# Kernel tuning notes

Measured on AMD Instinct MI355X. Metric: run time of the kernel, lower is better.

Reference implementation:

```python
import jax, jax.numpy as jnp
import numpy as np

B, T, C = 4, 2048, 1024
H, D = 16, 64          # n_head, head_size; H*D == C
FF = 4 * C             # compute_layer_scaling * n_embed
EPS = 1e-5


def layernorm(x, g, b):
    mu = jnp.mean(x, axis=-1, keepdims=True)
    var = jnp.var(x, axis=-1, keepdims=True)
    return (x - mu) * jax.lax.rsqrt(var + EPS) * g + b


def setup_inputs() -> dict:
    key = jax.random.key(0)
    ks = jax.random.split(key, 12)
    s_c = 1.0 / np.sqrt(C)
    s_ff = 1.0 / np.sqrt(FF)
    return {
        "x": jax.random.normal(ks[0], (B, T, C), dtype=jnp.float32),
        # per-head Q/K/V weights, stacked: [H, C, D] (Linear with bias=False)
        "Wq": jax.random.normal(ks[1], (H, C, D), dtype=jnp.float32) * s_c,
        "Wk": jax.random.normal(ks[2], (H, C, D), dtype=jnp.float32) * s_c,
        "Wv": jax.random.normal(ks[3], (H, C, D), dtype=jnp.float32) * s_c,
        "Wproj": jax.random.normal(ks[4], (C, C), dtype=jnp.float32) * s_c,
        "bproj": jnp.zeros((C,), dtype=jnp.float32),
        "W1": jax.random.normal(ks[5], (C, FF), dtype=jnp.float32) * s_c,
        "b1": jnp.zeros((FF,), dtype=jnp.float32),
        "W2": jax.random.normal(ks[6], (FF, FF), dtype=jnp.float32) * s_ff,
        "b2": jnp.zeros((FF,), dtype=jnp.float32),
        "W3": jax.random.normal(ks[7], (FF, C), dtype=jnp.float32) * s_ff,
        "b3": jnp.zeros((C,), dtype=jnp.float32),
        "ln1_g": jnp.ones((C,), dtype=jnp.float32),
        "ln1_b": jnp.zeros((C,), dtype=jnp.float32),
        "ln2_g": jnp.ones((C,), dtype=jnp.float32),
        "ln2_b": jnp.zeros((C,), dtype=jnp.float32),
    }


def reference(x, Wq, Wk, Wv, Wproj, bproj, W1, b1, W2, b2, W3, b3,
              ln1_g, ln1_b, ln2_g, ln2_b):
    # --- multi-head causal self-attention (pre-LN) ---
    h = layernorm(x, ln1_g, ln1_b)
    q = jnp.einsum("btc,hcd->bhtd", h, Wq)
    k = jnp.einsum("btc,hcd->bhtd", h, Wk)
    v = jnp.einsum("btc,hcd->bhtd", h, Wv)
    # NOTE: original scales by n_embed**-0.5 (C from x.shape), not head_size
    scores = jnp.einsum("bhtd,bhsd->bhts", q, k) * (C ** -0.5)
    causal = jnp.tril(jnp.ones((T, T), dtype=bool))
    scores = jnp.where(causal, scores, -jnp.inf)
    wei = jax.nn.softmax(scores, axis=-1)          # dropout p=0 -> identity
    attn = jnp.einsum("bhts,bhsd->bhtd", wei, v)
    attn = attn.transpose(0, 2, 1, 3).reshape(B, T, C)  # concat heads
    x = x + attn @ Wproj + bproj
    # --- feed-forward (pre-LN): C -> FF -> relu -> FF -> relu -> C ---
    h2 = layernorm(x, ln2_g, ln2_b)
    h2 = jax.nn.relu(h2 @ W1 + b1)
    h2 = jax.nn.relu(h2 @ W2 + b2)
    x = x + h2 @ W3 + b3
    return x
```

## Files before the change

kernel.cpp:

```cpp
#include <hip/hip_runtime.h>

typedef __bf16 bf16;
typedef bf16  bf16x8 __attribute__((ext_vector_type(8)));
typedef bf16  bf16x4 __attribute__((ext_vector_type(4)));
typedef float f32x4  __attribute__((ext_vector_type(4)));

#define T_SEQ 2048

__device__ __forceinline__ void gload_lds16(const bf16* g, bf16* l) {
    __builtin_amdgcn_global_load_lds(
        (const __attribute__((address_space(1))) unsigned int*)g,
        (__attribute__((address_space(3))) unsigned int*)l,
        16, 0, 0);
}

#define VMCNT(n) asm volatile("s_waitcnt vmcnt(" #n ")" ::: "memory")
#define BAR() do { asm volatile("" ::: "memory"); __builtin_amdgcn_s_barrier(); \
                   asm volatile("" ::: "memory"); } while (0)

__global__ __launch_bounds__(256) void transpose_f32_bf16(
    const float* __restrict__ in, bf16* __restrict__ out, int R, int Cc, int ldo)
{
    __shared__ float tile[32][33];
    const int bx = blockIdx.x * 32;
    const int by = blockIdx.y * 32;
    const long bi = (long)blockIdx.z * R * Cc;
    const long bo = (long)blockIdx.z * Cc * ldo;
    const int tx = threadIdx.x, ty = threadIdx.y;
#pragma unroll
    for (int i = 0; i < 4; ++i)
        tile[ty + i * 8][tx] = in[bi + (long)(by + ty + i * 8) * Cc + bx + tx];
    __syncthreads();
#pragma unroll
    for (int i = 0; i < 4; ++i)
        out[bo + (long)(bx + ty + i * 8) * ldo + by + tx] = (bf16)tile[tx][ty + i * 8];
}

__global__ __launch_bounds__(256) void ln_kernel(
    const float* __restrict__ x, const float* __restrict__ g,
    const float* __restrict__ bb, bf16* __restrict__ out)
{
    const long row = blockIdx.x;
    const int tid = threadIdx.x;
    const float4 v = ((const float4*)(x + row * 1024))[tid];
    float s  = v.x + v.y + v.z + v.w;
    float s2 = v.x * v.x + v.y * v.y + v.z * v.z + v.w * v.w;
#pragma unroll
    for (int off = 32; off >= 1; off >>= 1) {
        s  += __shfl_xor(s,  off, 64);
        s2 += __shfl_xor(s2, off, 64);
    }
    __shared__ float red[8];
    const int wid = tid >> 6;
    if ((tid & 63) == 0) { red[wid] = s; red[4 + wid] = s2; }
    __syncthreads();
    s  = red[0] + red[1] + red[2] + red[3];
    s2 = red[4] + red[5] + red[6] + red[7];
    const float mu   = s * (1.f / 1024.f);
    const float rstd = rsqrtf(s2 * (1.f / 1024.f) - mu * mu + 1e-5f);
    const float4 gv = ((const float4*)g)[tid];
    const float4 bv = ((const float4*)bb)[tid];
    bf16x4 ov;
    ov[0] = (bf16)((v.x - mu) * rstd * gv.x + bv.x);
    ov[1] = (bf16)((v.y - mu) * rstd * gv.y + bv.y);
    ov[2] = (bf16)((v.z - mu) * rstd * gv.z + bv.z);
    ov[3] = (bf16)((v.w - mu) * rstd * gv.w + bv.w);
    *(bf16x4*)(out + row * 1024 + tid * 4) = ov;
}

template <int MODE>
__global__ __launch_bounds__(256) void gemm_bt(
    const bf16* __restrict__ A, const bf16* __restrict__ Bt,
    const float* __restrict__ bias, const float* __restrict__ resid,
    void* __restrict__ outp, int M, int N, int K)
{
    __shared__ __align__(16) bf16 As[128 * 32];
    __shared__ __align__(16) bf16 Bs[128 * 32];
    const int tid = threadIdx.x;
    const int wid = tid >> 6, lane = tid & 63;
    const int wr = wid >> 1, wc = wid & 1;
    const int fr = lane & 15, fq = lane >> 4;
    const long bm = blockIdx.x, bn = blockIdx.y;

    const int c0   = wid * 2;
    const int row0 = c0 * 16 + (lane >> 2);
    const int kk8  = (lane & 3) * 8;
    const bf16* gA0 = A  + ((long)(bm * 128 + row0)) * K + kk8;
    const bf16* gA1 = gA0 + 16l * K;
    const bf16* gB0 = Bt + ((long)(bn * 128 + row0)) * K + kk8;
    const bf16* gB1 = gB0 + 16l * K;
    bf16* lA0 = &As[c0 * 512];
    bf16* lA1 = &As[(c0 + 1) * 512];
    bf16* lB0 = &Bs[c0 * 512];
    bf16* lB1 = &Bs[(c0 + 1) * 512];

    f32x4 acc[4][4];
#pragma unroll
    for (int m = 0; m < 4; ++m)
#pragma unroll
        for (int n = 0; n < 4; ++n) acc[m][n] = {0.f, 0.f, 0.f, 0.f};

    for (int k0 = 0; k0 < K; k0 += 32) {
        __syncthreads();
        gload_lds16(gA0 + k0, lA0);
        gload_lds16(gA1 + k0, lA1);
        gload_lds16(gB0 + k0, lB0);
        gload_lds16(gB1 + k0, lB1);
        __syncthreads();
        bf16x8 af[4], bfr[4];
#pragma unroll
        for (int m = 0; m < 4; ++m)
            af[m] = *(const bf16x8*)&As[(wr * 64 + m * 16 + fr) * 32 + fq * 8];
#pragma unroll
        for (int n = 0; n < 4; ++n)
            bfr[n] = *(const bf16x8*)&Bs[(wc * 64 + n * 16 + fr) * 32 + fq * 8];
#pragma unroll
        for (int m = 0; m < 4; ++m)
#pragma unroll
            for (int n = 0; n < 4; ++n)
                acc[m][n] = __builtin_amdgcn_mfma_f32_16x16x32_bf16(
                    af[m], bfr[n], acc[m][n], 0, 0, 0);
    }

#pragma unroll
    for (int m = 0; m < 4; ++m) {
        const long row0o = bm * 128 + wr * 64 + m * 16 + fq * 4;
#pragma unroll
        for (int n = 0; n < 4; ++n) {
            const long col = bn * 128 + wc * 64 + n * 16 + fr;
            const float bv = (MODE == 0) ? 0.f : bias[col];
#pragma unroll
            for (int j = 0; j < 4; ++j) {
                const long row = row0o + j;
                float v = acc[m][n][j] + bv;
                if (MODE == 1) v = fmaxf(v, 0.f);
                if (MODE == 2) {
                    v += resid[row * N + col];
                    ((float*)outp)[row * N + col] = v;
                } else {
                    ((bf16*)outp)[row * N + col] = (bf16)v;
                }
            }
        }
    }
}

#define LOADA(BUFP, QM) do {                                                   \
    const char* ab_ = (BUFP) + (size_t)((wr * 64 + (QM) * 128 + fr) * 128);    \
    _Pragma("unroll") for (int m_ = 0; m_ < 4; ++m_) {                         \
        af[m_][0] = *(const bf16x8*)(ab_ + m_ * 2048 + so0);                   \
        af[m_][1] = *(const bf16x8*)(ab_ + m_ * 2048 + so1); } } while (0)

#define LOADB(BUFP, QN) do {                                                   \
    const char* bb_ = (BUFP) + (size_t)((wc * 32 + (QN) * 128 + fr) * 128);    \
    _Pragma("unroll") for (int n_ = 0; n_ < 2; ++n_) {                         \
        bfv[n_][0] = *(const bf16x8*)(bb_ + n_ * 2048 + so0);                  \
        bfv[n_][1] = *(const bf16x8*)(bb_ + n_ * 2048 + so1); } } while (0)

#define MMA(ACC) do { __builtin_amdgcn_s_setprio(1);                           \
    _Pragma("unroll") for (int m_ = 0; m_ < 4; ++m_)                           \
    _Pragma("unroll") for (int n_ = 0; n_ < 2; ++n_) {                         \
        ACC[m_][n_] = __builtin_amdgcn_mfma_f32_16x16x32_bf16(                 \
            af[m_][0], bfv[n_][0], ACC[m_][n_], 0, 0, 0);                      \
        ACC[m_][n_] = __builtin_amdgcn_mfma_f32_16x16x32_bf16(                 \
            af[m_][1], bfv[n_][1], ACC[m_][n_], 0, 0, 0); }                    \
    __builtin_amdgcn_s_setprio(0); } while (0)

#define TILE_BODY(PRE) do {                                                    \
    const char* abuf = cAs + ((size_t)cur << 15);                              \
    const char* bbuf = cBs + ((size_t)cur << 15);                              \
    const long kn = (long)(k + 1) * 64;                                        \
    LOADA(abuf, 0);                                                            \
    LOADB(bbuf, 0);                                                            \
    if (PRE) { stageA(nxt, 0, kn); VMCNT(4); } else { VMCNT(2); }              \
    BAR(); MMA(a00); BAR();                                                    \
    LOADB(bbuf, 1);                                                            \
    if (PRE) { stageB(nxt, 0, kn); VMCNT(4); } else { VMCNT(0); }              \
    BAR(); MMA(a01); BAR();                                                    \
    LOADA(abuf, 1);                                                            \
    if (PRE) { stageB(nxt, 1, kn); }                                           \
    BAR(); MMA(a11); BAR();                                                    \
    LOADB(bbuf, 0);                                                            \
    if (PRE) { stageA(nxt, 1, kn); VMCNT(4); }                                 \
    BAR(); MMA(a10); BAR(); } while (0)

template <int MODE>
__global__ __launch_bounds__(512, 2) void gemm256(
    const bf16* __restrict__ A, const bf16* __restrict__ Bt,
    const float* __restrict__ bias, const float* __restrict__ resid,
    void* __restrict__ outp, int M, int N, int K, int nbn)
{
    extern __shared__ __align__(16) char smem[];
    char* cAs = smem;
    char* cBs = smem + 65536;

    const int tid = threadIdx.x;
    const int wid = tid >> 6, lane = tid & 63;
    const int wr = wid >> 2, wc = wid & 3;
    const int fr = lane & 15, fq = lane >> 4;

    const int nwg = gridDim.x;
    const int cpx = nwg >> 3;
    const int b0  = blockIdx.x;
    const int bid = (b0 & 7) * cpx + (b0 >> 3);
    const long bm = bid / nbn, bn = bid % nbn;
    const long bmrow = bm * 256, bnrow = bn * 256;

    const int srow0 = wid * 8 + (lane >> 3);
    const int sslot = (lane & 7) ^ (lane >> 3);
    auto stageA = [&](int buf, int h, long kt) {
        const bf16* g = A + (size_t)(bmrow + h * 128 + srow0) * K + kt + sslot * 8;
        char* l = cAs + ((size_t)buf << 15) + h * 16384 + (size_t)wid * 1024;
        gload_lds16(g, (bf16*)l);
        gload_lds16(g + (size_t)64 * K, (bf16*)(l + 8192));
    };
    auto stageB = [&](int buf, int h, long kt) {
        const bf16* g = Bt + (size_t)(bnrow + h * 128 + srow0) * K + kt + sslot * 8;
        char* l = cBs + ((size_t)buf << 15) + h * 16384 + (size_t)wid * 1024;
        gload_lds16(g, (bf16*)l);
        gload_lds16(g + (size_t)64 * K, (bf16*)(l + 8192));
    };

    const int sx  = fr & 7;
    const int so0 = ((fq) ^ sx) * 16;
    const int so1 = ((4 + fq) ^ sx) * 16;

    bf16x8 af[4][2], bfv[2][2];
    f32x4 a00[4][2], a01[4][2], a11[4][2], a10[4][2];
#pragma unroll
    for (int m = 0; m < 4; ++m)
#pragma unroll
        for (int n = 0; n < 2; ++n) {
            a00[m][n] = {0.f, 0.f, 0.f, 0.f}; a01[m][n] = {0.f, 0.f, 0.f, 0.f};
            a11[m][n] = {0.f, 0.f, 0.f, 0.f}; a10[m][n] = {0.f, 0.f, 0.f, 0.f};
        }

    stageA(0, 0, 0); stageB(0, 0, 0); stageB(0, 1, 0); stageA(0, 1, 0);
    VMCNT(4);
    BAR();

    const int NT = K >> 6;
    int cur = 0, nxt = 1;
    int k = 0;
    for (; k < NT - 1; ++k) {
        cur = k & 1; nxt = cur ^ 1;
        TILE_BODY(true);
    }
    cur = k & 1; nxt = cur ^ 1;
    TILE_BODY(false);

    auto writeQ = [&](f32x4 (&acc)[4][2], int QM, int QN) {
#pragma unroll
        for (int m = 0; m < 4; ++m) {
            const long row0 = bmrow + wr * 64 + QM * 128 + m * 16 + fq * 4;
#pragma unroll
            for (int n = 0; n < 2; ++n) {
                const long col = bnrow + wc * 32 + QN * 128 + n * 16 + fr;
                const float bv = (MODE == 0) ? 0.f : bias[col];
#pragma unroll
                for (int j = 0; j < 4; ++j) {
                    const long row = row0 + j;
                    float v = acc[m][n][j] + bv;
                    if (MODE == 1) v = fmaxf(v, 0.f);
                    if (MODE == 2) {
                        v += resid[row * N + col];
                        ((float*)outp)[row * N + col] = v;
                    } else {
                        ((bf16*)outp)[row * N + col] = (bf16)v;
                    }
                }
            }
        }
    };
    writeQ(a00, 0, 0); writeQ(a01, 0, 1); writeQ(a11, 1, 1); writeQ(a10, 1, 0);
}

__device__ __forceinline__ void attn_step(
    const bf16* __restrict__ Ks, const bf16* __restrict__ Vt,
    bf16* __restrict__ Pp, const bf16x8* qf,
    f32x4* o, float* mj, float* lj,
    int fr, int fq, int qloc, bool diag)
{
    f32x4 s[4];
#pragma unroll
    for (int n = 0; n < 4; ++n) s[n] = {0.f, 0.f, 0.f, 0.f};
#pragma unroll
    for (int n = 0; n < 4; ++n) {
        const int t  = n * 16 + fr;
        const int sw = ((t ^ (t >> 3)) & 7) << 4;
#pragma unroll
        for (int kk = 0; kk < 2; ++kk) {
            const bf16x8 kf = *(const bf16x8*)((const char*)Ks + t * 128
                                               + ((kk * 64 + fq * 16) ^ sw));
            s[n] = __builtin_amdgcn_mfma_f32_16x16x32_bf16(qf[kk], kf, s[n], 0, 0, 0);
        }
    }
#pragma unroll
    for (int j = 0; j < 4; ++j) {
        const int qg = qloc + fq * 4 + j;
        float v0 = s[0][j] * 0.03125f, v1 = s[1][j] * 0.03125f;
        float v2 = s[2][j] * 0.03125f, v3 = s[3][j] * 0.03125f;
        if (diag) {
            if (fr      > qg) v0 = -1e30f;
            if (16 + fr > qg) v1 = -1e30f;
            if (32 + fr > qg) v2 = -1e30f;
            if (48 + fr > qg) v3 = -1e30f;
        }
        float mx = fmaxf(fmaxf(v0, v1), fmaxf(v2, v3));
#pragma unroll
        for (int off = 1; off <= 8; off <<= 1) mx = fmaxf(mx, __shfl_xor(mx, off, 16));
        const float mn   = fmaxf(mj[j], mx);
        const float corr = __expf(mj[j] - mn);
        mj[j] = mn;
        v0 = __expf(v0 - mn); v1 = __expf(v1 - mn);
        v2 = __expf(v2 - mn); v3 = __expf(v3 - mn);
        float r = v0 + v1 + v2 + v3;
#pragma unroll
        for (int off = 1; off <= 8; off <<= 1) r += __shfl_xor(r, off, 16);
        lj[j] = lj[j] * corr + r;
#pragma unroll
        for (int nd = 0; nd < 4; ++nd) o[nd][j] *= corr;
        bf16* prow = Pp + (fq * 4 + j) * 72;
        prow[fr]      = (bf16)v0;
        prow[16 + fr] = (bf16)v1;
        prow[32 + fr] = (bf16)v2;
        prow[48 + fr] = (bf16)v3;
    }
    asm volatile("s_waitcnt lgkmcnt(0)" ::: "memory");
    __builtin_amdgcn_sched_barrier(0);
    const bf16x8 pf0 = *(const bf16x8*)(Pp + fr * 72 + fq * 8);
    const bf16x8 pf1 = *(const bf16x8*)(Pp + fr * 72 + 32 + fq * 8);
#pragma unroll
    for (int nd = 0; nd < 4; ++nd) {
        const int dd = nd * 16 + fr;
        const int sw = ((dd ^ (dd >> 3)) & 7) << 4;
        const bf16x8 vf0 = *(const bf16x8*)((const char*)Vt + dd * 128 + ((fq * 16) ^ sw));
        const bf16x8 vf1 = *(const bf16x8*)((const char*)Vt + dd * 128 + ((64 + fq * 16) ^ sw));
        o[nd] = __builtin_amdgcn_mfma_f32_16x16x32_bf16(pf0, vf0, o[nd], 0, 0, 0);
        o[nd] = __builtin_amdgcn_mfma_f32_16x16x32_bf16(pf1, vf1, o[nd], 0, 0, 0);
    }
}

__global__ __launch_bounds__(256) void attn_kernel(
    const bf16* __restrict__ qkv, bf16* __restrict__ out)
{
    const int pair = blockIdx.x;
    const int h = blockIdx.y, b = blockIdx.z;
    const int tid = threadIdx.x, wid = tid >> 6, lane = tid & 63;
    const int fr = lane & 15, fq = lane >> 4;
    const int jA = pair, jB = 31 - pair;
    const bf16* base = qkv + ((long)b * T_SEQ) * 3072 + h * 64;

    __shared__ __align__(16) bf16 Ks[64 * 64];
    __shared__ __align__(16) bf16 Vt[64 * 64];
    __shared__ __align__(16) bf16 Plds[2][4][16 * 72];

    const int qrA = jA * 64 + wid * 16 + fr;
    const int qrB = jB * 64 + wid * 16 + fr;
    bf16x8 qfA[2], qfB[2];
#pragma unroll
    for (int kk = 0; kk < 2; ++kk) {
        qfA[kk] = *(const bf16x8*)(base + (long)qrA * 3072 + kk * 32 + fq * 8);
        qfB[kk] = *(const bf16x8*)(base + (long)qrB * 3072 + kk * 32 + fq * 8);
    }

    f32x4 oA[4], oB[4];
    float mA[4], lAv[4], mB[4], lBv[4];
#pragma unroll
    for (int nd = 0; nd < 4; ++nd) { oA[nd] = {0.f, 0.f, 0.f, 0.f}; oB[nd] = {0.f, 0.f, 0.f, 0.f}; }
#pragma unroll
    for (int j = 0; j < 4; ++j) { mA[j] = -1e30f; lAv[j] = 0.f; mB[j] = -1e30f; lBv[j] = 0.f; }

    const int t_p0 = wid * 16 + (lane >> 3);
    const int t_p1 = t_p0 + 8;
    const int kcb0 = ((lane & 7) * 16) ^ (((t_p0 ^ (t_p0 >> 3)) & 7) << 4);
    const int kcb1 = ((lane & 7) * 16) ^ (((t_p1 ^ (t_p1 >> 3)) & 7) << 4);
    bf16* lK0 = &Ks[(wid * 2) * 512];
    bf16* lK1 = &Ks[(wid * 2 + 1) * 512];
    const int vtok = tid >> 3;
    const int vd0  = (tid & 7) * 8;

    bf16* PA = &Plds[0][wid][0];
    bf16* PB = &Plds[1][wid][0];

    const int nch = jB + 1;
    for (int c = 0; c < nch; ++c) {
        const int s0 = c * 64;
        const bf16* vsrc = base + (long)(s0 + vtok) * 3072 + 2048 + vd0;
        const bf16x8 vv0 = *(const bf16x8*)vsrc;
        const bf16x8 vv1 = *(const bf16x8*)(vsrc + 32l * 3072);
        __syncthreads();
        gload_lds16(base + (long)(s0 + t_p0) * 3072 + 1024 + (kcb0 >> 1), lK0);
        gload_lds16(base + (long)(s0 + t_p1) * 3072 + 1024 + (kcb1 >> 1), lK1);
#pragma unroll
        for (int e = 0; e < 8; ++e) {
            const int d  = vd0 + e;
            const int sw = ((d ^ (d >> 3)) & 7) << 4;
            *(bf16*)((char*)Vt + ((d * 128 + vtok * 2) ^ sw))        = vv0[e];
            *(bf16*)((char*)Vt + ((d * 128 + (vtok + 32) * 2) ^ sw)) = vv1[e];
        }
        __syncthreads();
        if (c <= jA)
            attn_step(Ks, Vt, PA, qfA, oA, mA, lAv, fr, fq, wid * 16, c == jA);
        attn_step(Ks, Vt, PB, qfB, oB, mB, lBv, fr, fq, wid * 16, c == jB);
    }

#pragma unroll
    for (int nd = 0; nd < 4; ++nd)
#pragma unroll
        for (int j = 0; j < 4; ++j) {
            const long rowA = (long)b * T_SEQ + jA * 64 + wid * 16 + fq * 4 + j;
            const long rowB = (long)b * T_SEQ + jB * 64 + wid * 16 + fq * 4 + j;
            out[rowA * 1024 + h * 64 + nd * 16 + fr] = (bf16)(oA[nd][j] / lAv[j]);
            out[rowB * 1024 + h * 64 + nd * 16 + fr] = (bf16)(oB[nd][j] / lBv[j]);
        }
}

extern "C" void kernel_launch(void* const* d_in, const int* in_sizes, int n_in,
                              void* d_out, int out_size, void* d_ws, size_t ws_size,
                              hipStream_t stream)
{
    const float* x     = (const float*)d_in[0];
    const float* Wq    = (const float*)d_in[1];
    const float* Wk    = (const float*)d_in[2];
    const float* Wv    = (const float*)d_in[3];
    const float* Wproj = (const float*)d_in[4];
    const float* bproj = (const float*)d_in[5];
    const float* W1    = (const float*)d_in[6];
    const float* b1    = (const float*)d_in[7];
    const float* W2    = (const float*)d_in[8];
    const float* b2    = (const float*)d_in[9];
    const float* W3    = (const float*)d_in[10];
    const float* b3    = (const float*)d_in[11];
    const float* ln1g  = (const float*)d_in[12];
    const float* ln1b  = (const float*)d_in[13];
    const float* ln2g  = (const float*)d_in[14];
    const float* ln2b  = (const float*)d_in[15];

    char* ws = (char*)d_ws;
    size_t off = 0;
    auto alloc = [&](size_t bytes) {
        void* p = ws + off;
        off += (bytes + 255) & ~(size_t)255;
        return p;
    };
    bf16* Wqkv_t  = (bf16*)alloc(3072ul * 1024 * 2);
    bf16* Wproj_t = (bf16*)alloc(1024ul * 1024 * 2);
    bf16* W1_t    = (bf16*)alloc(4096ul * 1024 * 2);
    bf16* W2_t    = (bf16*)alloc(4096ul * 4096 * 2);
    bf16* W3_t    = (bf16*)alloc(1024ul * 4096 * 2);
    bf16* hbuf    = (bf16*)alloc(8192ul * 1024 * 2);
    float* x1     = (float*)alloc(8192ul * 1024 * 4);
    bf16* a1      = (bf16*)alloc(8192ul * 4096 * 2);
    char* R1      = (char*)alloc(8192ul * 4096 * 2);
    bf16* qkvb    = (bf16*)R1;
    bf16* attnb   = (bf16*)(R1 + 8192ul * 3072 * 2);
    bf16* a2      = (bf16*)R1;

    hipFuncSetAttribute(reinterpret_cast<const void*>(&gemm256<0>),
                        hipFuncAttributeMaxDynamicSharedMemorySize, 131072);
    hipFuncSetAttribute(reinterpret_cast<const void*>(&gemm256<1>),
                        hipFuncAttributeMaxDynamicSharedMemorySize, 131072);

    const dim3 tb(32, 8);
    transpose_f32_bf16<<<dim3(2, 32, 16), tb, 0, stream>>>(Wq, Wqkv_t,                1024, 64, 1024);
    transpose_f32_bf16<<<dim3(2, 32, 16), tb, 0, stream>>>(Wk, Wqkv_t + 1024l * 1024, 1024, 64, 1024);
    transpose_f32_bf16<<<dim3(2, 32, 16), tb, 0, stream>>>(Wv, Wqkv_t + 2048l * 1024, 1024, 64, 1024);
    transpose_f32_bf16<<<dim3(32, 32, 1),   tb, 0, stream>>>(Wproj, Wproj_t, 1024, 1024, 1024);
    transpose_f32_bf16<<<dim3(128, 32, 1),  tb, 0, stream>>>(W1, W1_t, 1024, 4096, 1024);
    transpose_f32_bf16<<<dim3(128, 128, 1), tb, 0, stream>>>(W2, W2_t, 4096, 4096, 4096);
    transpose_f32_bf16<<<dim3(32, 128, 1),  tb, 0, stream>>>(W3, W3_t, 4096, 1024, 4096);

    ln_kernel<<<8192, 256, 0, stream>>>(x, ln1g, ln1b, hbuf);
    gemm256<0><<<384, 512, 131072, stream>>>(hbuf, Wqkv_t, nullptr, nullptr, qkvb,
                                             8192, 3072, 1024, 12);
    attn_kernel<<<dim3(16, 16, 4), 256, 0, stream>>>(qkvb, attnb);
    gemm_bt<2><<<dim3(64, 8), 256, 0, stream>>>(attnb, Wproj_t, bproj, x, x1, 8192, 1024, 1024);
    ln_kernel<<<8192, 256, 0, stream>>>(x1, ln2g, ln2b, hbuf);
    gemm256<1><<<512, 512, 131072, stream>>>(hbuf, W1_t, b1, nullptr, a1,
                                             8192, 4096, 1024, 16);
    gemm256<1><<<512, 512, 131072, stream>>>(a1, W2_t, b2, nullptr, a2,
                                             8192, 4096, 4096, 16);
    gemm_bt<2><<<dim3(64, 8), 256, 0, stream>>>(a2, W3_t, b3, x1, (float*)d_out, 8192, 1024, 4096);
}
```

Measured before the change: 735.4 us.

## Use pipelined 256x128 GEMM for narrow outputs and lazy softmax rescaling in attention

Adds a double-buffered 256x128-tile GEMM kernel (gemm256n) and uses it in place of the simple 128x128 gemm_bt for the projection and W3 GEMMs, and in place of the 256x256 kernel for the QKV GEMM. The goal is better load overlap and more workgroups on the narrow-N GEMMs. In attention, the running max is only rescaled when some row's max grows by more than 8, and the row sum is accumulated by an MFMA against a ones vector instead of shuffle reductions. Together these cut VALU and shuffle work in softmax. The cost is extra MFMA work and less headroom against overflow when the max is stale.

After: 704.7 us. -4.2%, faster.

```diff
diff --git a/kernel.cpp b/kernel.cpp
--- a/kernel.cpp
+++ b/kernel.cpp
@@ -66,83 +66,6 @@
     ov[2] = (bf16)((v.z - mu) * rstd * gv.z + bv.z);
     ov[3] = (bf16)((v.w - mu) * rstd * gv.w + bv.w);
     *(bf16x4*)(out + row * 1024 + tid * 4) = ov;
-}
-
-template <int MODE>
-__global__ __launch_bounds__(256) void gemm_bt(
-    const bf16* __restrict__ A, const bf16* __restrict__ Bt,
-    const float* __restrict__ bias, const float* __restrict__ resid,
-    void* __restrict__ outp, int M, int N, int K)
-{
-    __shared__ __align__(16) bf16 As[128 * 32];
-    __shared__ __align__(16) bf16 Bs[128 * 32];
-    const int tid = threadIdx.x;
-    const int wid = tid >> 6, lane = tid & 63;
-    const int wr = wid >> 1, wc = wid & 1;
-    const int fr = lane & 15, fq = lane >> 4;
-    const long bm = blockIdx.x, bn = blockIdx.y;
-
-    const int c0   = wid * 2;
-    const int row0 = c0 * 16 + (lane >> 2);
-    const int kk8  = (lane & 3) * 8;
-    const bf16* gA0 = A  + ((long)(bm * 128 + row0)) * K + kk8;
-    const bf16* gA1 = gA0 + 16l * K;
-    const bf16* gB0 = Bt + ((long)(bn * 128 + row0)) * K + kk8;
-    const bf16* gB1 = gB0 + 16l * K;
-    bf16* lA0 = &As[c0 * 512];
-    bf16* lA1 = &As[(c0 + 1) * 512];
-    bf16* lB0 = &Bs[c0 * 512];
-    bf16* lB1 = &Bs[(c0 + 1) * 512];
-
-    f32x4 acc[4][4];
-#pragma unroll
-    for (int m = 0; m < 4; ++m)
-#pragma unroll
-        for (int n = 0; n < 4; ++n) acc[m][n] = {0.f, 0.f, 0.f, 0.f};
-
-    for (int k0 = 0; k0 < K; k0 += 32) {
-        __syncthreads();
-        gload_lds16(gA0 + k0, lA0);
-        gload_lds16(gA1 + k0, lA1);
-        gload_lds16(gB0 + k0, lB0);
-        gload_lds16(gB1 + k0, lB1);
-        __syncthreads();
-        bf16x8 af[4], bfr[4];
-#pragma unroll
-        for (int m = 0; m < 4; ++m)
-            af[m] = *(const bf16x8*)&As[(wr * 64 + m * 16 + fr) * 32 + fq * 8];
-#pragma unroll
-        for (int n = 0; n < 4; ++n)
-            bfr[n] = *(const bf16x8*)&Bs[(wc * 64 + n * 16 + fr) * 32 + fq * 8];
-#pragma unroll
-        for (int m = 0; m < 4; ++m)
-#pragma unroll
-            for (int n = 0; n < 4; ++n)
-                acc[m][n] = __builtin_amdgcn_mfma_f32_16x16x32_bf16(
-                    af[m], bfr[n], acc[m][n], 0, 0, 0);
-    }
-
-#pragma unroll
-    for (int m = 0; m < 4; ++m) {
-        const long row0o = bm * 128 + wr * 64 + m * 16 + fq * 4;
-#pragma unroll
-        for (int n = 0; n < 4; ++n) {
-            const long col = bn * 128 + wc * 64 + n * 16 + fr;
-            const float bv = (MODE == 0) ? 0.f : bias[col];
-#pragma unroll
-            for (int j = 0; j < 4; ++j) {
-                const long row = row0o + j;
-                float v = acc[m][n][j] + bv;
-                if (MODE == 1) v = fmaxf(v, 0.f);
-                if (MODE == 2) {
-                    v += resid[row * N + col];
-                    ((float*)outp)[row * N + col] = v;
-                } else {
-                    ((bf16*)outp)[row * N + col] = (bf16)v;
-                }
-            }
-        }
-    }
 }
 
 #define LOADA(BUFP, QM) do {                                                   \
@@ -275,10 +198,115 @@
     writeQ(a00, 0, 0); writeQ(a01, 0, 1); writeQ(a11, 1, 1); writeQ(a10, 1, 0);
 }
 
+#define TILE_BODY_N(PRE, LAST) do {                                            \
+    const char* abuf = cAs + ((size_t)cur << 15);                              \
+    const char* bbuf = cBs + ((size_t)cur << 14);                              \
+    const long kn = (long)(k + 1) * 64;                                        \
+    LOADA(abuf, 0);                                                            \
+    LOADB(bbuf, 0);                                                            \
+    if (PRE) { stageA(nxt, 0, kn); VMCNT(2); } else { VMCNT(0); }              \
+    BAR(); MMA(aq0); BAR();                                                    \
+    LOADA(abuf, 1);                                                            \
+    if (PRE) { stageB(nxt, kn); stageA(nxt, 1, kn); VMCNT(2); }                \
+    if (!LAST) { BAR(); }                                                      \
+    MMA(aq1);                                                                  \
+    if (!LAST) { BAR(); } } while (0)
+
+template <int MODE>
+__global__ __launch_bounds__(512, 2) void gemm256n(
+    const bf16* __restrict__ A, const bf16* __restrict__ Bt,
+    const float* __restrict__ bias, const float* __restrict__ resid,
+    void* __restrict__ outp, int M, int N, int K, int nbn)
+{
+    extern __shared__ __align__(16) char smem[];
+    char* cAs = smem;
+    char* cBs = smem + 65536;
+
+    const int tid = threadIdx.x;
+    const int wid = tid >> 6, lane = tid & 63;
+    const int wr = wid >> 2, wc = wid & 3;
+    const int fr = lane & 15, fq = lane >> 4;
+
+    const int nwg = gridDim.x;
+    const int cpx = nwg >> 3;
+    const int b0  = blockIdx.x;
+    const int bid = (b0 & 7) * cpx + (b0 >> 3);
+    const long bm = bid / nbn, bn = bid % nbn;
+    const long bmrow = bm * 256, bnrow = bn * 128;
+
+    const int srow0 = wid * 8 + (lane >> 3);
+    const int sslot = (lane & 7) ^ (lane >> 3);
+    auto stageA = [&](int buf, int h, long kt) {
+        const bf16* g = A + (size_t)(bmrow + h * 128 + srow0) * K + kt + sslot * 8;
+        char* l = cAs + ((size_t)buf << 15) + h * 16384 + (size_t)wid * 1024;
+        gload_lds16(g, (bf16*)l);
+        gload_lds16(g + (size_t)64 * K, (bf16*)(l + 8192));
+    };
+    auto stageB = [&](int buf, long kt) {
+        const bf16* g = Bt + (size_t)(bnrow + srow0) * K + kt + sslot * 8;
+        char* l = cBs + ((size_t)buf << 14) + (size_t)wid * 1024;
+        gload_lds16(g, (bf16*)l);
+        gload_lds16(g + (size_t)64 * K, (bf16*)(l + 8192));
+    };
+
+    const int sx  = fr & 7;
+    const int so0 = ((fq) ^ sx) * 16;
+    const int so1 = ((4 + fq) ^ sx) * 16;
+
+    bf16x8 af[4][2], bfv[2][2];
+    f32x4 aq0[4][2], aq1[4][2];
+#pragma unroll
+    for (int m = 0; m < 4; ++m)
+#pragma unroll
+        for (int n = 0; n < 2; ++n) {
+            aq0[m][n] = {0.f, 0.f, 0.f, 0.f};
+            aq1[m][n] = {0.f, 0.f, 0.f, 0.f};
+        }
+
+    stageA(0, 0, 0); stageB(0, 0); stageA(0, 1, 0);
+    VMCNT(2);
+    BAR();
+
+    const int NT = K >> 6;
+    int cur = 0, nxt = 1;
+    int k = 0;
+    for (; k < NT - 1; ++k) {
+        cur = k & 1; nxt = cur ^ 1;
+        TILE_BODY_N(true, false);
+    }
+    cur = k & 1; nxt = cur ^ 1;
+    TILE_BODY_N(false, true);
+
+    auto writeQ = [&](f32x4 (&acc)[4][2], int QM) {
+#pragma unroll
+        for (int m = 0; m < 4; ++m) {
+            const long row0 = bmrow + wr * 64 + QM * 128 + m * 16 + fq * 4;
+#pragma unroll
+            for (int n = 0; n < 2; ++n) {
+                const long col = bnrow + wc * 32 + n * 16 + fr;
+                const float bv = (MODE == 0) ? 0.f : bias[col];
+#pragma unroll
+                for (int j = 0; j < 4; ++j) {
+                    const long row = row0 + j;
+                    float v = acc[m][n][j] + bv;
+                    if (MODE == 1) v = fmaxf(v, 0.f);
+                    if (MODE == 2) {
+                        v += resid[row * N + col];
+                        ((float*)outp)[row * N + col] = v;
+                    } else {
+                        ((bf16*)outp)[row * N + col] = (bf16)v;
+                    }
+                }
+            }
+        }
+    };
+    writeQ(aq0, 0); writeQ(aq1, 1);
+}
+
 __device__ __forceinline__ void attn_step(
     const bf16* __restrict__ Ks, const bf16* __restrict__ Vt,
     bf16* __restrict__ Pp, const bf16x8* qf,
-    f32x4* o, float* mj, float* lj,
+    f32x4* o, f32x4& o_l, float* mj, const bf16x8 onesf,
     int fr, int fq, int qloc, bool diag)
 {
     f32x4 s[4];
@@ -295,36 +323,47 @@
             s[n] = __builtin_amdgcn_mfma_f32_16x16x32_bf16(qf[kk], kf, s[n], 0, 0, 0);
         }
     }
+    float v[4][4], mxj[4];
 #pragma unroll
     for (int j = 0; j < 4; ++j) {
         const int qg = qloc + fq * 4 + j;
-        float v0 = s[0][j] * 0.03125f, v1 = s[1][j] * 0.03125f;
-        float v2 = s[2][j] * 0.03125f, v3 = s[3][j] * 0.03125f;
+        v[0][j] = s[0][j] * 0.03125f;
+        v[1][j] = s[1][j] * 0.03125f;
+        v[2][j] = s[2][j] * 0.03125f;
+        v[3][j] = s[3][j] * 0.03125f;
         if (diag) {
-            if (fr      > qg) v0 = -1e30f;
-            if (16 + fr > qg) v1 = -1e30f;
-            if (32 + fr > qg) v2 = -1e30f;
-            if (48 + fr > qg) v3 = -1e30f;
-        }
-        float mx = fmaxf(fmaxf(v0, v1), fmaxf(v2, v3));
+            if (fr      > qg) v[0][j] = -1e30f;
+            if (16 + fr > qg) v[1][j] = -1e30f;
+            if (32 + fr > qg) v[2][j] = -1e30f;
+            if (48 + fr > qg) v[3][j] = -1e30f;
+        }
+        float mx = fmaxf(fmaxf(v[0][j], v[1][j]), fmaxf(v[2][j], v[3][j]));
 #pragma unroll
         for (int off = 1; off <= 8; off <<= 1) mx = fmaxf(mx, __shfl_xor(mx, off, 16));
-        const float mn   = fmaxf(mj[j], mx);
-        const float corr = __expf(mj[j] - mn);
-        mj[j] = mn;
-        v0 = __expf(v0 - mn); v1 = __expf(v1 - mn);
-        v2 = __expf(v2 - mn); v3 = __expf(v3 - mn);
-        float r = v0 + v1 + v2 + v3;
-#pragma unroll
-        for (int off = 1; off <= 8; off <<= 1) r += __shfl_xor(r, off, 16);
-        lj[j] = lj[j] * corr + r;
-#pragma unroll
-        for (int nd = 0; nd < 4; ++nd) o[nd][j] *= corr;
+        mxj[j] = mx;
+    }
+    float need = mxj[0] - mj[0];
+    need = fmaxf(need, mxj[1] - mj[1]);
+    need = fmaxf(need, mxj[2] - mj[2]);
+    need = fmaxf(need, mxj[3] - mj[3]);
+    if (__any(need > 8.f)) {
+#pragma unroll
+        for (int j = 0; j < 4; ++j) {
+            const float mn   = fmaxf(mj[j], mxj[j]);
+            const float corr = __expf(mj[j] - mn);
+            mj[j] = mn;
+#pragma unroll
+            for (int nd = 0; nd < 4; ++nd) o[nd][j] *= corr;
+            o_l[j] *= corr;
+        }
+    }
+#pragma unroll
+    for (int j = 0; j < 4; ++j) {
         bf16* prow = Pp + (fq * 4 + j) * 72;
-        prow[fr]      = (bf16)v0;
-        prow[16 + fr] = (bf16)v1;
-        prow[32 + fr] = (bf16)v2;
-        prow[48 + fr] = (bf16)v3;
+        prow[fr]      = (bf16)__expf(v[0][j] - mj[j]);
+        prow[16 + fr] = (bf16)__expf(v[1][j] - mj[j]);
+        prow[32 + fr] = (bf16)__expf(v[2][j] - mj[j]);
+        prow[48 + fr] = (bf16)__expf(v[3][j] - mj[j]);
     }
     asm volatile("s_waitcnt lgkmcnt(0)" ::: "memory");
     __builtin_amdgcn_sched_barrier(0);
@@ -339,6 +378,8 @@
         o[nd] = __builtin_amdgcn_mfma_f32_16x16x32_bf16(pf0, vf0, o[nd], 0, 0, 0);
         o[nd] = __builtin_amdgcn_mfma_f32_16x16x32_bf16(pf1, vf1, o[nd], 0, 0, 0);
     }
+    o_l = __builtin_amdgcn_mfma_f32_16x16x32_bf16(pf0, onesf, o_l, 0, 0, 0);
+    o_l = __builtin_amdgcn_mfma_f32_16x16x32_bf16(pf1, onesf, o_l, 0, 0, 0);
 }
 
 __global__ __launch_bounds__(256) void attn_kernel(
@@ -364,12 +405,20 @@
         qfB[kk] = *(const bf16x8*)(base + (long)qrB * 3072 + kk * 32 + fq * 8);
     }
 
-    f32x4 oA[4], oB[4];
-    float mA[4], lAv[4], mB[4], lBv[4];
+    bf16x8 onesf;
+    {
+        const bf16 ov = (fr == 0) ? (bf16)1.f : (bf16)0.f;
+#pragma unroll
+        for (int e = 0; e < 8; ++e) onesf[e] = ov;
+    }
+
+    f32x4 oA[4], oB[4], olA, olB;
+    float mA[4], mB[4];
 #pragma unroll
     for (int nd = 0; nd < 4; ++nd) { oA[nd] = {0.f, 0.f, 0.f, 0.f}; oB[nd] = {0.f, 0.f, 0.f, 0.f}; }
-#pragma unroll
-    for (int j = 0; j < 4; ++j) { mA[j] = -1e30f; lAv[j] = 0.f; mB[j] = -1e30f; lBv[j] = 0.f; }
+    olA = {0.f, 0.f, 0.f, 0.f}; olB = {0.f, 0.f, 0.f, 0.f};
+#pragma unroll
+    for (int j = 0; j < 4; ++j) { mA[j] = -1e30f; mB[j] = -1e30f; }
 
     const int t_p0 = wid * 16 + (lane >> 3);
     const int t_p1 = t_p0 + 8;
@@ -401,19 +450,23 @@
         }
         __syncthreads();
         if (c <= jA)
-            attn_step(Ks, Vt, PA, qfA, oA, mA, lAv, fr, fq, wid * 16, c == jA);
-        attn_step(Ks, Vt, PB, qfB, oB, mB, lBv, fr, fq, wid * 16, c == jB);
-    }
-
-#pragma unroll
-    for (int nd = 0; nd < 4; ++nd)
-#pragma unroll
-        for (int j = 0; j < 4; ++j) {
-            const long rowA = (long)b * T_SEQ + jA * 64 + wid * 16 + fq * 4 + j;
-            const long rowB = (long)b * T_SEQ + jB * 64 + wid * 16 + fq * 4 + j;
-            out[rowA * 1024 + h * 64 + nd * 16 + fr] = (bf16)(oA[nd][j] / lAv[j]);
-            out[rowB * 1024 + h * 64 + nd * 16 + fr] = (bf16)(oB[nd][j] / lBv[j]);
-        }
+            attn_step(Ks, Vt, PA, qfA, oA, olA, mA, onesf, fr, fq, wid * 16, c == jA);
+        attn_step(Ks, Vt, PB, qfB, oB, olB, mB, onesf, fr, fq, wid * 16, c == jB);
+    }
+
+#pragma unroll
+    for (int j = 0; j < 4; ++j) {
+        const float lA = __shfl(olA[j], lane & 48, 64);
+        const float lB = __shfl(olB[j], lane & 48, 64);
+        const float rA = 1.f / lA, rB = 1.f / lB;
+        const long rowA = (long)b * T_SEQ + jA * 64 + wid * 16 + fq * 4 + j;
+        const long rowB = (long)b * T_SEQ + jB * 64 + wid * 16 + fq * 4 + j;
+#pragma unroll
+        for (int nd = 0; nd < 4; ++nd) {
+            out[rowA * 1024 + h * 64 + nd * 16 + fr] = (bf16)(oA[nd][j] * rA);
+            out[rowB * 1024 + h * 64 + nd * 16 + fr] = (bf16)(oB[nd][j] * rB);
+        }
+    }
 }
 
 extern "C" void kernel_launch(void* const* d_in, const int* in_sizes, int n_in,
@@ -457,10 +510,12 @@
     bf16* attnb   = (bf16*)(R1 + 8192ul * 3072 * 2);
     bf16* a2      = (bf16*)R1;
 
-    hipFuncSetAttribute(reinterpret_cast<const void*>(&gemm256<0>),
-                        hipFuncAttributeMaxDynamicSharedMemorySize, 131072);
     hipFuncSetAttribute(reinterpret_cast<const void*>(&gemm256<1>),
                         hipFuncAttributeMaxDynamicSharedMemorySize, 131072);
+    hipFuncSetAttribute(reinterpret_cast<const void*>(&gemm256n<0>),
+                        hipFuncAttributeMaxDynamicSharedMemorySize, 98304);
+    hipFuncSetAttribute(reinterpret_cast<const void*>(&gemm256n<2>),
+                        hipFuncAttributeMaxDynamicSharedMemorySize, 98304);
 
     const dim3 tb(32, 8);
     transpose_f32_bf16<<<dim3(2, 32, 16), tb, 0, stream>>>(Wq, Wqkv_t,                1024, 64, 1024);
@@ -472,14 +527,16 @@
     transpose_f32_bf16<<<dim3(32, 128, 1),  tb, 0, stream>>>(W3, W3_t, 4096, 1024, 4096);
 
     ln_kernel<<<8192, 256, 0, stream>>>(x, ln1g, ln1b, hbuf);
-    gemm256<0><<<384, 512, 131072, stream>>>(hbuf, Wqkv_t, nullptr, nullptr, qkvb,
-                                             8192, 3072, 1024, 12);
+    gemm256n<0><<<768, 512, 98304, stream>>>(hbuf, Wqkv_t, nullptr, nullptr, qkvb,
+                                             8192, 3072, 1024, 24);
     attn_kernel<<<dim3(16, 16, 4), 256, 0, stream>>>(qkvb, attnb);
-    gemm_bt<2><<<dim3(64, 8), 256, 0, stream>>>(attnb, Wproj_t, bproj, x, x1, 8192, 1024, 1024);
+    gemm256n<2><<<256, 512, 98304, stream>>>(attnb, Wproj_t, bproj, x, x1,
+                                             8192, 1024, 1024, 8);
     ln_kernel<<<8192, 256, 0, stream>>>(x1, ln2g, ln2b, hbuf);
     gemm256<1><<<512, 512, 131072, stream>>>(hbuf, W1_t, b1, nullptr, a1,
                                              8192, 4096, 1024, 16);
     gemm256<1><<<512, 512, 131072, stream>>>(a1, W2_t, b2, nullptr, a2,
                                              8192, 4096, 4096, 16);
-    gemm_bt<2><<<dim3(64, 8), 256, 0, stream>>>(a2, W3_t, b3, x1, (float*)d_out, 8192, 1024, 4096);
-}
+    gemm256n<2><<<256, 512, 98304, stream>>>(a2, W3_t, b3, x1, (float*)d_out,
+                                             8192, 1024, 4096, 8);
+}
```
